# Kernel tuning notes

Hardware: AMD Instinct MI355X
Metric: run time of the kernel (lower is better)

The kernel has to match this reference:

```python
import jax, jax.numpy as jnp
import numpy as np

EPS = 1e-6
SCALING = 32 ** -0.5  # key_dim ** -0.5


def _ln(x, g, b):
    m = jnp.mean(x, -1, keepdims=True)
    v = jnp.var(x, -1, keepdims=True)
    return (x - m) * jax.lax.rsqrt(v + EPS) * g + b


def _dwconv(x, w, b, pad):
    # x: (B,H,W,C); w: (kh,kw,1,C) depthwise kernel
    y = jax.lax.conv_general_dilated(
        x, w, (1, 1), [(pad, pad), (pad, pad)],
        dimension_numbers=("NHWC", "HWIO", "NHWC"),
        feature_group_count=x.shape[-1])
    return y + b


def _rotate_every_two(x):
    x1 = x[..., ::2]
    x2 = x[..., 1::2]
    return jnp.stack([-x2, x1], axis=-1).reshape(x.shape)


def _theta_shift(x, sin, cos):
    return x * cos + _rotate_every_two(x) * sin


def setup_inputs() -> dict:
    key = jax.random.key(0)
    ks = jax.random.split(key, 32)
    B, H, W, C = 2, 56, 56, 256
    N, D = 8, C // 8          # heads, key_dim
    F = 1024                  # ffn_dim
    L = H * W
    g = 2 ** -2.5
    inp = {
        "x": jax.random.normal(ks[0], (B, H, W, C), jnp.float32),
        "sin": jax.random.normal(ks[1], (H, W, D), jnp.float32),
        "cos": jax.random.normal(ks[2], (H, W, D), jnp.float32),
        "mask": jax.random.normal(ks[3], (N, L, L), jnp.float32),
        # pos dwconv 3x3
        "pos_w": jax.random.normal(ks[4], (3, 3, 1, C), jnp.float32) * 0.05,
        "pos_b": jnp.zeros((C,), jnp.float32),
        # retention layernorm
        "ln1_g": jnp.ones((C,), jnp.float32),
        "ln1_b": jnp.zeros((C,), jnp.float32),
        # q/k/v projections (stored as (in,out))
        "wq": jax.random.normal(ks[5], (C, C), jnp.float32) * g * (2.0 / (C + C)) ** 0.5 * 10,
        "bq": jnp.zeros((C,), jnp.float32),
        "wk": jax.random.normal(ks[6], (C, C), jnp.float32) * g * 0.06,
        "bk": jnp.zeros((C,), jnp.float32),
        "wv": jax.random.normal(ks[7], (C, C), jnp.float32) * g * 0.06,
        "bv": jnp.zeros((C,), jnp.float32),
        # lepe dwconv 5x5
        "lepe_w": jax.random.normal(ks[8], (5, 5, 1, C), jnp.float32) * 0.05,
        "lepe_b": jnp.zeros((C,), jnp.float32),
        # out proj
        "wo": jax.random.normal(ks[9], (C, C), jnp.float32) * 0.06,
        "bo": jnp.zeros((C,), jnp.float32),
        # final layernorm
        "ln2_g": jnp.ones((C,), jnp.float32),
        "ln2_b": jnp.zeros((C,), jnp.float32),
        # ffn
        "w1": jax.random.normal(ks[10], (C, F), jnp.float32) * 0.04,
        "b1": jnp.zeros((F,), jnp.float32),
        "ffn_w": jax.random.normal(ks[11], (3, 3, 1, F), jnp.float32) * 0.05,
        "ffn_b": jnp.zeros((F,), jnp.float32),
        "w2": jax.random.normal(ks[12], (F, C), jnp.float32) * 0.04,
        "b2": jnp.zeros((C,), jnp.float32),
    }
    return inp


def _forward(x, sin, cos, mask, pos_w, pos_b, ln1_g, ln1_b, wq, bq, wk, bk,
             wv, bv, lepe_w, lepe_b, wo, bo, ln2_g, ln2_b, w1, b1,
             ffn_w, ffn_b, w2, b2):
    B, H, W, C = x.shape
    N = mask.shape[0]
    D = C // N
    L = H * W

    # positional dwconv residual
    x = x + _dwconv(x, pos_w, pos_b, 1)

    # ---- retention (VisionRetentionAll) ----
    y = _ln(x, ln1_g, ln1_b)
    q = y @ wq + bq
    k = (y @ wk + bk) * SCALING
    v = y @ wv + bv
    lepe = _dwconv(v, lepe_w, lepe_b, 2)

    # (B,H,W,C) -> (B,N,H,W,D)
    q = q.reshape(B, H, W, N, D).transpose(0, 3, 1, 2, 4)
    k = k.reshape(B, H, W, N, D).transpose(0, 3, 1, 2, 4)
    qr = _theta_shift(q, sin, cos).reshape(B, N, L, D)
    kr = _theta_shift(k, sin, cos).reshape(B, N, L, D)
    vr = v.reshape(B, H, W, N, D).transpose(0, 3, 1, 2, 4).reshape(B, N, L, D)

    qk = jnp.einsum("bnld,bnmd->bnlm", qr, kr) + mask  # (B,N,L,L)
    att = jax.nn.softmax(qk, axis=-1)
    out = jnp.einsum("bnlm,bnmd->bnld", att, vr)       # (B,N,L,D)
    out = out.transpose(0, 2, 1, 3).reshape(B, H, W, C)
    out = (out + lepe) @ wo + bo
    x = x + out

    # ---- FFN with depthwise conv ----
    z = _ln(x, ln2_g, ln2_b)
    z = jax.nn.gelu(z @ w1 + b1, approximate=False)
    z = z + _dwconv(z, ffn_w, ffn_b, 1)
    z = z @ w2 + b2
    return x + z


def reference(x, sin, cos, mask, pos_w, pos_b, ln1_g, ln1_b, wq, bq, wk, bk,
              wv, bv, lepe_w, lepe_b, wo, bo, ln2_g, ln2_b, w1, b1,
              ffn_w, ffn_b, w2, b2):
    return _forward(x, sin, cos, mask, pos_w, pos_b, ln1_g, ln1_b, wq, bq,
                    wk, bk, wv, bv, lepe_w, lepe_b, wo, bo, ln2_g, ln2_b,
                    w1, b1, ffn_w, ffn_b, w2, b2)
```

## Files before the change

kernel.cpp:

```cpp
#include <hip/hip_runtime.h>
#include <hip/hip_bf16.h>
#include <math.h>

#define Bn 2
#define Hn 56
#define Wn 56
#define Cn 256
#define Nh 8
#define Dh 32
#define Fn 1024
#define Ln (Hn*Wn)
#define Mrows (Bn*Ln)
#define SCALING_K 0.17677669529663687f

typedef __attribute__((ext_vector_type(4))) float f32x4;
typedef __attribute__((ext_vector_type(8))) short s16x8;
typedef unsigned short ushort_t;

__device__ __forceinline__ ushort_t f2bf(float f) {
    __hip_bfloat16 h = __float2bfloat16(f);
    return *reinterpret_cast<ushort_t*>(&h);
}

__global__ __launch_bounds__(256) void transpose_w(
    const float* __restrict__ wq, const float* __restrict__ wk, const float* __restrict__ wv,
    const float* __restrict__ wo, const float* __restrict__ w1, const float* __restrict__ w2,
    ushort_t* __restrict__ wqkvT, ushort_t* __restrict__ woT,
    ushort_t* __restrict__ w1T, ushort_t* __restrict__ w2T)
{
    int z = blockIdx.z;
    const float* src; ushort_t* dst; int K, N; float scale = 1.f;
    switch (z) {
      case 0: src=wq; dst=wqkvT;           K=256;  N=256;  break;
      case 1: src=wk; dst=wqkvT+256*256;   K=256;  N=256;  scale=SCALING_K; break;
      case 2: src=wv; dst=wqkvT+512*256;   K=256;  N=256;  break;
      case 3: src=wo; dst=woT;             K=256;  N=256;  break;
      case 4: src=w1; dst=w1T;             K=256;  N=1024; break;
      default: src=w2; dst=w2T;            K=1024; N=256;  break;
    }
    int n0 = blockIdx.x << 5, k0 = blockIdx.y << 5;
    if (n0 >= N || k0 >= K) return;
    __shared__ float tile[32][33];
    int tx = threadIdx.x & 31, ty = threadIdx.x >> 5;
    #pragma unroll
    for (int r = 0; r < 4; ++r)
        tile[ty + 8*r][tx] = src[(size_t)(k0 + ty + 8*r)*N + n0 + tx] * scale;
    __syncthreads();
    #pragma unroll
    for (int r = 0; r < 4; ++r)
        dst[(size_t)(n0 + ty + 8*r)*K + k0 + tx] = f2bf(tile[tx][ty + 8*r]);
}

__global__ void prep_bias(const float* __restrict__ bq, const float* __restrict__ bk,
                          const float* __restrict__ bv, float* __restrict__ bqkv)
{
    int i = blockIdx.x*256 + threadIdx.x;
    if (i < 768)
        bqkv[i] = (i < 256) ? bq[i] : (i < 512 ? bk[i-256]*SCALING_K : bv[i-512]);
}

__global__ __launch_bounds__(256) void dwconv_ln(
    const float* __restrict__ x, const float* __restrict__ wgt, const float* __restrict__ bias,
    float* __restrict__ out, float2* __restrict__ stats)
{
    int t = threadIdx.x;
    int cg = t & 63;
    int g = blockIdx.x*4 + (t >> 6);
    int w0 = (g % 14) << 2;
    int hr = g / 14;
    int h = hr % Hn;
    int c = cg << 2;
    float4 wv9[9];
    #pragma unroll
    for (int i = 0; i < 9; ++i) wv9[i] = *(const float4*)&wgt[i*Cn + c];
    float4 bias4 = *(const float4*)&bias[c];
    float4 acc[4] = {bias4, bias4, bias4, bias4};
    const float* base = x + (size_t)(hr - h)*Wn*Cn + c;
    #pragma unroll
    for (int dh = 0; dh < 3; ++dh) {
        int hh = h + dh - 1;
        if (hh < 0 || hh >= Hn) continue;
        const float* rowp = base + (size_t)hh*Wn*Cn;
        float4 xv[6];
        #pragma unroll
        for (int j = 0; j < 6; ++j) {
            int wc = w0 - 1 + j;
            xv[j] = (wc >= 0 && wc < Wn) ? *(const float4*)&rowp[(size_t)wc*Cn]
                                         : make_float4(0.f,0.f,0.f,0.f);
        }
        #pragma unroll
        for (int dw = 0; dw < 3; ++dw) {
            float4 wv = wv9[dh*3 + dw];
            #pragma unroll
            for (int p = 0; p < 4; ++p) {
                acc[p].x += xv[p+dw].x*wv.x; acc[p].y += xv[p+dw].y*wv.y;
                acc[p].z += xv[p+dw].z*wv.z; acc[p].w += xv[p+dw].w*wv.w;
            }
        }
        if (dh == 1) {
            #pragma unroll
            for (int p = 0; p < 4; ++p) {
                acc[p].x += xv[p+1].x; acc[p].y += xv[p+1].y;
                acc[p].z += xv[p+1].z; acc[p].w += xv[p+1].w;
            }
        }
    }
    float s[4], q[4];
    #pragma unroll
    for (int p = 0; p < 4; ++p) {
        s[p] = acc[p].x + acc[p].y + acc[p].z + acc[p].w;
        q[p] = acc[p].x*acc[p].x + acc[p].y*acc[p].y + acc[p].z*acc[p].z + acc[p].w*acc[p].w;
    }
    #pragma unroll
    for (int m = 1; m < 64; m <<= 1) {
        #pragma unroll
        for (int p = 0; p < 4; ++p) {
            s[p] += __shfl_xor(s[p], m);
            q[p] += __shfl_xor(q[p], m);
        }
    }
    size_t pixbase = (size_t)hr*Wn + w0;
    #pragma unroll
    for (int p = 0; p < 4; ++p)
        *(float4*)&out[(pixbase + p)*Cn + c] = acc[p];
    if (cg == 0) {
        #pragma unroll
        for (int p = 0; p < 4; ++p) {
            float mean = s[p] * (1.0f/Cn);
            float var  = q[p] * (1.0f/Cn) - mean*mean;
            stats[pixbase + p] = make_float2(mean, rsqrtf(var + 1e-6f));
        }
    }
}

template<int KS, int OBF>
__global__ __launch_bounds__(256) void dwconv4(
    const float* __restrict__ in, const float* __restrict__ wgt, const float* __restrict__ bias,
    void* __restrict__ outv, int C, int inld, int addin)
{
    constexpr int PAD = KS/2;
    int t = threadIdx.x;
    int cgs = C >> 2;
    int qpb = 256 / cgs;
    int cg = t % cgs;
    int g = blockIdx.x*qpb + t/cgs;
    int w0 = (g % 14) << 2;
    int hr = g / 14;
    int h = hr % Hn;
    int c = cg << 2;
    float4 bias4 = *(const float4*)&bias[c];
    float4 acc[4] = {bias4, bias4, bias4, bias4};
    const float* base = in + (size_t)(hr - h)*Wn*inld + c;
    #pragma unroll
    for (int dh = 0; dh < KS; ++dh) {
        int hh = h + dh - PAD;
        if (hh < 0 || hh >= Hn) continue;
        const float* rowp = base + (size_t)hh*Wn*inld;
        float4 xv[KS+3];
        #pragma unroll
        for (int j = 0; j < KS+3; ++j) {
            int wc = w0 - PAD + j;
            xv[j] = (wc >= 0 && wc < Wn) ? *(const float4*)&rowp[(size_t)wc*inld]
                                         : make_float4(0.f,0.f,0.f,0.f);
        }
        #pragma unroll
        for (int dw = 0; dw < KS; ++dw) {
            float4 wv = *(const float4*)&wgt[(dh*KS + dw)*C + c];
            #pragma unroll
            for (int p = 0; p < 4; ++p) {
                acc[p].x += xv[p+dw].x*wv.x; acc[p].y += xv[p+dw].y*wv.y;
                acc[p].z += xv[p+dw].z*wv.z; acc[p].w += xv[p+dw].w*wv.w;
            }
        }
        if (addin && dh == PAD) {
            #pragma unroll
            for (int p = 0; p < 4; ++p) {
                acc[p].x += xv[p+PAD].x; acc[p].y += xv[p+PAD].y;
                acc[p].z += xv[p+PAD].z; acc[p].w += xv[p+PAD].w;
            }
        }
    }
    size_t pixbase = (size_t)hr*Wn + w0;
    if (OBF) {
        ushort_t* outb = (ushort_t*)outv;
        #pragma unroll
        for (int p = 0; p < 4; ++p) {
            ushort_t tmp[4] = { f2bf(acc[p].x), f2bf(acc[p].y), f2bf(acc[p].z), f2bf(acc[p].w) };
            *(uint2*)&outb[(pixbase + p)*C + c] = *(uint2*)tmp;
        }
    } else {
        float* outf = (float*)outv;
        #pragma unroll
        for (int p = 0; p < 4; ++p)
            *(float4*)&outf[(pixbase + p)*C + c] = acc[p];
    }
}

__global__ __launch_bounds__(256) void ln_stats(const float* __restrict__ in, float2* __restrict__ stats)
{
    int row = blockIdx.x;
    int t = threadIdx.x;
    float v = in[(size_t)row*Cn + t];
    float s1 = v, s2 = v*v;
    #pragma unroll
    for (int m = 1; m < 64; m <<= 1) {
        s1 += __shfl_xor(s1, m);
        s2 += __shfl_xor(s2, m);
    }
    __shared__ float w1s[4], w2s[4];
    if ((t & 63) == 0) { w1s[t>>6] = s1; w2s[t>>6] = s2; }
    __syncthreads();
    if (t == 0) {
        s1 = w1s[0]+w1s[1]+w1s[2]+w1s[3];
        s2 = w2s[0]+w2s[1]+w2s[2]+w2s[3];
        float mean = s1 * (1.0f/Cn);
        float var  = s2 * (1.0f/Cn) - mean*mean;
        stats[row] = make_float2(mean, rsqrtf(var + 1e-6f));
    }
}

__global__ __launch_bounds__(256) void gemm_bf16(
    const void* __restrict__ Av, int abf16, const float* __restrict__ A2, int lda,
    const float2* __restrict__ lnstat, const float* __restrict__ lng, const float* __restrict__ lnb,
    const ushort_t* __restrict__ BT, const float* __restrict__ bias,
    const float* __restrict__ resid, float* __restrict__ out, int ldo,
    int K, int gelu_flag)
{
    __shared__ __align__(16) ushort_t As[64][40];
    __shared__ __align__(16) ushort_t Bs[64][40];
    int t = threadIdx.x;
    int wid = t >> 6, lane = t & 63, l16 = lane & 15, quad = lane >> 4;
    int n0 = blockIdx.x << 6, m0 = blockIdx.y << 6;
    int srow = t >> 2, skc = (t & 3) << 3;
    float2 st = make_float2(0.f, 1.f);
    if (lnstat) st = lnstat[m0 + srow];
    f32x4 acc[4] = {{0,0,0,0},{0,0,0,0},{0,0,0,0},{0,0,0,0}};
    for (int k0 = 0; k0 < K; k0 += 32) {
        ushort_t ac[8];
        if (abf16) {
            *(uint4*)ac = *(const uint4*)&((const ushort_t*)Av)[(size_t)(m0+srow)*lda + k0 + skc];
        } else {
            float av[8];
            const float* ap = &((const float*)Av)[(size_t)(m0+srow)*lda + k0 + skc];
            *(float4*)&av[0] = *(const float4*)ap;
            *(float4*)&av[4] = *(const float4*)(ap + 4);
            if (A2) {
                const float* ap2 = &A2[(size_t)(m0+srow)*lda + k0 + skc];
                float4 x0 = *(const float4*)ap2;
                float4 x1 = *(const float4*)(ap2 + 4);
                av[0]+=x0.x; av[1]+=x0.y; av[2]+=x0.z; av[3]+=x0.w;
                av[4]+=x1.x; av[5]+=x1.y; av[6]+=x1.z; av[7]+=x1.w;
            }
            if (lnstat) {
                float gg[8], bb[8];
                *(float4*)&gg[0] = *(const float4*)&lng[k0 + skc];
                *(float4*)&gg[4] = *(const float4*)&lng[k0 + skc + 4];
                *(float4*)&bb[0] = *(const float4*)&lnb[k0 + skc];
                *(float4*)&bb[4] = *(const float4*)&lnb[k0 + skc + 4];
                #pragma unroll
                for (int i = 0; i < 8; ++i)
                    av[i] = (av[i] - st.x)*st.y*gg[i] + bb[i];
            }
            #pragma unroll
            for (int i = 0; i < 8; ++i) ac[i] = f2bf(av[i]);
        }
        uint4 bv4 = *(const uint4*)&BT[(size_t)(n0+srow)*K + k0 + skc];
        __syncthreads();
        *(uint4*)&As[srow][skc] = *(uint4*)ac;
        *(uint4*)&Bs[srow][skc] = bv4;
        __syncthreads();
        s16x8 af = *(const s16x8*)&As[wid*16 + l16][quad*8];
        #pragma unroll
        for (int j = 0; j < 4; ++j) {
            s16x8 bf = *(const s16x8*)&Bs[j*16 + l16][quad*8];
            acc[j] = __builtin_amdgcn_mfma_f32_16x16x32_bf16(af, bf, acc[j], 0, 0, 0);
        }
    }
    #pragma unroll
    for (int j = 0; j < 4; ++j) {
        int col = n0 + j*16 + l16;
        float bv = bias[col];
        #pragma unroll
        for (int r = 0; r < 4; ++r) {
            int row = m0 + wid*16 + quad*4 + r;
            float v = acc[j][r] + bv;
            if (gelu_flag) v = 0.5f * v * (1.0f + erff(v * 0.70710678118654752f));
            size_t off = (size_t)row*ldo + col;
            if (resid) v += resid[off];
            out[off] = v;
        }
    }
}

__global__ __launch_bounds__(256) void pack_qkv(
    const float* __restrict__ qkv,
    const float* __restrict__ sp, const float* __restrict__ cp,
    ushort_t* __restrict__ qb, ushort_t* __restrict__ kb, ushort_t* __restrict__ vbT)
{
    __shared__ __align__(16) ushort_t Vl[64][40];
    int t = threadIdx.x;
    int l0 = blockIdx.x << 6;
    int n = blockIdx.y;
    int b = blockIdx.z;
    {
        int ll = t >> 2, dc = (t & 3) << 3;
        int l = l0 + ll;
        size_t gbase = ((size_t)(b*Ln + l))*768 + n*Dh + dc;
        float qx[8], kx[8], vx[8], sv[8], cv[8];
        *(float4*)&qx[0] = *(const float4*)&qkv[gbase];
        *(float4*)&qx[4] = *(const float4*)&qkv[gbase+4];
        *(float4*)&kx[0] = *(const float4*)&qkv[gbase+256];
        *(float4*)&kx[4] = *(const float4*)&qkv[gbase+260];
        *(float4*)&vx[0] = *(const float4*)&qkv[gbase+512];
        *(float4*)&vx[4] = *(const float4*)&qkv[gbase+516];
        size_t scb = (size_t)l*Dh + dc;
        *(float4*)&sv[0] = *(const float4*)&sp[scb];
        *(float4*)&sv[4] = *(const float4*)&sp[scb+4];
        *(float4*)&cv[0] = *(const float4*)&cp[scb];
        *(float4*)&cv[4] = *(const float4*)&cp[scb+4];
        ushort_t qo[8], ko[8], vo[8];
        #pragma unroll
        for (int j = 0; j < 8; j += 2) {
            float q0 = qx[j]*cv[j] - qx[j+1]*sv[j];
            float q1 = qx[j+1]*cv[j+1] + qx[j]*sv[j+1];
            float k0 = kx[j]*cv[j] - kx[j+1]*sv[j];
            float k1 = kx[j+1]*cv[j+1] + kx[j]*sv[j+1];
            qo[j] = f2bf(q0); qo[j+1] = f2bf(q1);
            ko[j] = f2bf(k0); ko[j+1] = f2bf(k1);
            vo[j] = f2bf(vx[j]); vo[j+1] = f2bf(vx[j+1]);
        }
        size_t hbase = ((size_t)((b*Nh + n)*Ln + l))*Dh + dc;
        *(uint4*)&qb[hbase] = *(uint4*)qo;
        *(uint4*)&kb[hbase] = *(uint4*)ko;
        *(uint4*)&Vl[ll][dc] = *(uint4*)vo;
    }
    __syncthreads();
    {
        int d = t >> 3, lc = (t & 7) << 3;
        ushort_t tmp[8];
        #pragma unroll
        for (int i = 0; i < 8; ++i) tmp[i] = Vl[lc + i][d];
        size_t tbase = ((size_t)((b*Nh + n)*Dh + d))*Ln + l0 + lc;
        *(uint4*)&vbT[tbase] = *(uint4*)tmp;
    }
}

__global__ __launch_bounds__(512) void flash_mfma(
    const ushort_t* __restrict__ qb, const ushort_t* __restrict__ kb,
    const ushort_t* __restrict__ vbT, const float* __restrict__ mask,
    float* __restrict__ out)
{
    __shared__ __align__(16) ushort_t Kt[2][64][40];
    __shared__ __align__(16) ushort_t Vt[2][32][72];
    __shared__ __align__(16) ushort_t Ps[8][16][72];
    int t = threadIdx.x;
    int wid = t >> 6, lane = t & 63, l16 = lane & 15, quad = lane >> 4;
    int bb = wid & 1, wq16 = wid >> 1;
    int l0 = blockIdx.x << 6;
    int n = blockIdx.y;

    const ushort_t* qbp = qb + ((size_t)(bb*Nh + n))*Ln*Dh;
    s16x8 qfrag = *(const s16x8*)(qbp + (size_t)(l0 + wq16*16 + l16)*Dh + quad*8);
    const float* mbase = mask + (size_t)n*Ln*Ln + (size_t)(l0 + wq16*16 + quad*4)*Ln;

    int sb   = t >> 8;
    int krow = (t >> 2) & 63, kkc = (t & 3) << 3;
    int vrow = (t >> 3) & 31, vkc = (t & 7) << 3;
    const ushort_t* kst = kb  + ((size_t)(sb*Nh + n))*Ln*Dh;
    const ushort_t* vst = vbT + ((size_t)((sb*Nh + n)*Dh + vrow))*Ln;

    f32x4 O0 = {0.f,0.f,0.f,0.f}, O1 = {0.f,0.f,0.f,0.f};
    float m_[4], l_[4];
    #pragma unroll
    for (int r = 0; r < 4; ++r) { m_[r] = -INFINITY; l_[r] = 0.f; }

    uint4 kreg = *(const uint4*)(kst + (size_t)krow*Dh + kkc);
    uint4 vreg = *(const uint4*)(vst + vkc);
    f32x4 c0, c1, c2, c3;
    #pragma unroll
    for (int r = 0; r < 4; ++r) {
        const float* mr = mbase + (size_t)r*Ln + l16;
        c0[r] = mr[0]; c1[r] = mr[16]; c2[r] = mr[32]; c3[r] = mr[48];
    }

    for (int m0 = 0; m0 < Ln; m0 += 64) {
        __syncthreads();
        *(uint4*)&Kt[sb][krow][kkc] = kreg;
        *(uint4*)&Vt[sb][vrow][vkc] = vreg;
        __syncthreads();

        int m1 = m0 + 64;
        uint4 krn = kreg, vrn = vreg;
        f32x4 d0 = c0, d1 = c1, d2 = c2, d3 = c3;
        if (m1 < Ln) {
            krn = *(const uint4*)(kst + (size_t)(m1 + krow)*Dh + kkc);
            vrn = *(const uint4*)(vst + m1 + vkc);
            #pragma unroll
            for (int r = 0; r < 4; ++r) {
                const float* mr = mbase + (size_t)r*Ln + m1 + l16;
                d0[r] = mr[0]; d1[r] = mr[16]; d2[r] = mr[32]; d3[r] = mr[48];
            }
        }

        f32x4 S[4];
        {
            s16x8 kf0 = *(const s16x8*)&Kt[bb][ 0 + l16][quad*8];
            s16x8 kf1 = *(const s16x8*)&Kt[bb][16 + l16][quad*8];
            s16x8 kf2 = *(const s16x8*)&Kt[bb][32 + l16][quad*8];
            s16x8 kf3 = *(const s16x8*)&Kt[bb][48 + l16][quad*8];
            S[0] = __builtin_amdgcn_mfma_f32_16x16x32_bf16(qfrag, kf0, c0, 0, 0, 0);
            S[1] = __builtin_amdgcn_mfma_f32_16x16x32_bf16(qfrag, kf1, c1, 0, 0, 0);
            S[2] = __builtin_amdgcn_mfma_f32_16x16x32_bf16(qfrag, kf2, c2, 0, 0, 0);
            S[3] = __builtin_amdgcn_mfma_f32_16x16x32_bf16(qfrag, kf3, c3, 0, 0, 0);
        }
        #pragma unroll
        for (int r = 0; r < 4; ++r) {
            float tm = fmaxf(fmaxf(S[0][r], S[1][r]), fmaxf(S[2][r], S[3][r]));
            tm = fmaxf(tm, __shfl_xor(tm, 1));
            tm = fmaxf(tm, __shfl_xor(tm, 2));
            tm = fmaxf(tm, __shfl_xor(tm, 4));
            tm = fmaxf(tm, __shfl_xor(tm, 8));
            float nm = fmaxf(m_[r], tm);
            float al = __expf(m_[r] - nm);
            m_[r] = nm;
            float p0 = __expf(S[0][r] - nm);
            float p1 = __expf(S[1][r] - nm);
            float p2 = __expf(S[2][r] - nm);
            float p3 = __expf(S[3][r] - nm);
            float ps = p0 + p1 + p2 + p3;
            ps += __shfl_xor(ps, 1); ps += __shfl_xor(ps, 2);
            ps += __shfl_xor(ps, 4); ps += __shfl_xor(ps, 8);
            l_[r] = l_[r]*al + ps;
            O0[r] *= al; O1[r] *= al;
            int rr = quad*4 + r;
            Ps[wid][rr][ 0 + l16] = f2bf(p0);
            Ps[wid][rr][16 + l16] = f2bf(p1);
            Ps[wid][rr][32 + l16] = f2bf(p2);
            Ps[wid][rr][48 + l16] = f2bf(p3);
        }
        #pragma unroll
        for (int kc = 0; kc < 2; ++kc) {
            s16x8 pf  = *(const s16x8*)&Ps[wid][l16][kc*32 + quad*8];
            s16x8 vf0 = *(const s16x8*)&Vt[bb][ 0 + l16][kc*32 + quad*8];
            s16x8 vf1 = *(const s16x8*)&Vt[bb][16 + l16][kc*32 + quad*8];
            O0 = __builtin_amdgcn_mfma_f32_16x16x32_bf16(pf, vf0, O0, 0, 0, 0);
            O1 = __builtin_amdgcn_mfma_f32_16x16x32_bf16(pf, vf1, O1, 0, 0, 0);
        }
        kreg = krn; vreg = vrn;
        c0 = d0; c1 = d1; c2 = d2; c3 = d3;
    }
    #pragma unroll
    for (int r = 0; r < 4; ++r) {
        float inv = 1.0f / l_[r];
        size_t row = (size_t)(bb*Ln + l0 + wq16*16 + quad*4 + r)*Cn + n*Dh;
        out[row + l16]      = O0[r] * inv;
        out[row + 16 + l16] = O1[r] * inv;
    }
}

extern "C" void kernel_launch(void* const* d_in, const int* in_sizes, int n_in,
                              void* d_out, int out_size, void* d_ws, size_t ws_size,
                              hipStream_t stream) {
    const float* x     = (const float*)d_in[0];
    const float* sinp  = (const float*)d_in[1];
    const float* cosp  = (const float*)d_in[2];
    const float* mask  = (const float*)d_in[3];
    const float* pos_w = (const float*)d_in[4];
    const float* pos_b = (const float*)d_in[5];
    const float* ln1_g = (const float*)d_in[6];
    const float* ln1_b = (const float*)d_in[7];
    const float* wq = (const float*)d_in[8];
    const float* bq = (const float*)d_in[9];
    const float* wk = (const float*)d_in[10];
    const float* bk = (const float*)d_in[11];
    const float* wv = (const float*)d_in[12];
    const float* bv = (const float*)d_in[13];
    const float* lepe_w = (const float*)d_in[14];
    const float* lepe_b = (const float*)d_in[15];
    const float* wo = (const float*)d_in[16];
    const float* bo = (const float*)d_in[17];
    const float* ln2_g = (const float*)d_in[18];
    const float* ln2_b = (const float*)d_in[19];
    const float* w1 = (const float*)d_in[20];
    const float* b1 = (const float*)d_in[21];
    const float* ffn_w = (const float*)d_in[22];
    const float* ffn_b = (const float*)d_in[23];
    const float* w2 = (const float*)d_in[24];
    const float* b2 = (const float*)d_in[25];

    float* ws = (float*)d_ws;
    const size_t MC = (size_t)Mrows*Cn;
    float* xbuf = ws;
    float* qkv  = ws + MC;
    float* lepe = ws + 4*MC;
    float* x2   = ws + 5*MC;
    float* att  = ws + 6*MC;
    float* z1   = ws + 7*MC;
    ushort_t* z2bf = (ushort_t*)(ws + 11*MC);
    ushort_t* qb   = (ushort_t*)(ws + 13*MC);
    ushort_t* kb   = (ushort_t*)(ws + 13*MC + MC/2);
    ushort_t* vbT  = (ushort_t*)(ws + 14*MC);
    float* wtb = ws + 14*MC + MC/2;
    ushort_t* wqkvT = (ushort_t*)wtb;
    ushort_t* woT   = (ushort_t*)(wtb + 98304);
    ushort_t* w1T   = (ushort_t*)(wtb + 131072);
    ushort_t* w2T   = (ushort_t*)(wtb + 262144);
    float*    bqkv  = wtb + 393216;
    float2*   stats1 = (float2*)(wtb + 394240);
    float2*   stats2 = (float2*)(wtb + 406784);
    float* outp = (float*)d_out;

    transpose_w<<<dim3(32,32,6), 256, 0, stream>>>(wq,wk,wv,wo,w1,w2, wqkvT,woT,w1T,w2T);
    prep_bias<<<3, 256, 0, stream>>>(bq,bk,bv,bqkv);
    dwconv_ln<<<Mrows/16, 256, 0, stream>>>(x, pos_w, pos_b, xbuf, stats1);
    gemm_bf16<<<dim3(12, Mrows/64), 256, 0, stream>>>(xbuf, 0, nullptr, Cn,
        stats1, ln1_g, ln1_b, wqkvT, bqkv, nullptr, qkv, 768, Cn, 0);
    pack_qkv<<<dim3(Ln/64, Nh, Bn), 256, 0, stream>>>(qkv, sinp, cosp, qb, kb, vbT);
    dwconv4<5,0><<<Mrows/16, 256, 0, stream>>>(qkv+512, lepe_w, lepe_b, lepe, Cn, 768, 0);
    flash_mfma<<<dim3(Ln/64, Nh), 512, 0, stream>>>(qb, kb, vbT, mask, att);
    gemm_bf16<<<dim3(4, Mrows/64), 256, 0, stream>>>(att, 0, lepe, Cn,
        nullptr, nullptr, nullptr, woT, bo, xbuf, x2, Cn, Cn, 0);
    ln_stats<<<Mrows, 256, 0, stream>>>(x2, stats2);
    gemm_bf16<<<dim3(16, Mrows/64), 256, 0, stream>>>(x2, 0, nullptr, Cn,
        stats2, ln2_g, ln2_b, w1T, b1, nullptr, z1, Fn, Cn, 1);
    dwconv4<3,1><<<Mrows/4, 256, 0, stream>>>(z1, ffn_w, ffn_b, z2bf, Fn, Fn, 1);
    gemm_bf16<<<dim3(4, Mrows/64), 256, 0, stream>>>(z2bf, 1, nullptr, Fn,
        nullptr, nullptr, nullptr, w2T, b2, x2, outp, Cn, Fn, 0);
}
```

Baseline: 655.3 us.

## Apply layernorm and lepe add upstream, feed GEMMs bf16 activations

The first layernorm is now applied inside the pos-dwconv kernel and the second in a new row kernel, both writing normalized bf16 activations. The flash attention epilogue adds lepe and stores bf16. The GEMM A-load path is therefore a plain bf16 copy with no per-tile LN math, fp32-to-bf16 conversion or second operand read. The workspace is repacked, with z1 aliasing the qkv region. This moves normalization work out of GEMM loops that recompute it for every N tile and halves A-side read traffic, at the cost of an extra bf16 write and read of each activation.

```diff
diff --git a/kernel.cpp b/kernel.cpp
--- a/kernel.cpp
+++ b/kernel.cpp
@@ -61,7 +61,8 @@
 
 __global__ __launch_bounds__(256) void dwconv_ln(
     const float* __restrict__ x, const float* __restrict__ wgt, const float* __restrict__ bias,
-    float* __restrict__ out, float2* __restrict__ stats)
+    const float* __restrict__ lng, const float* __restrict__ lnb,
+    float* __restrict__ out, ushort_t* __restrict__ ybf)
 {
     int t = threadIdx.x;
     int cg = t & 63;
@@ -119,17 +120,21 @@
             q[p] += __shfl_xor(q[p], m);
         }
     }
+    float4 g4 = *(const float4*)&lng[c];
+    float4 b4 = *(const float4*)&lnb[c];
     size_t pixbase = (size_t)hr*Wn + w0;
     #pragma unroll
-    for (int p = 0; p < 4; ++p)
+    for (int p = 0; p < 4; ++p) {
         *(float4*)&out[(pixbase + p)*Cn + c] = acc[p];
-    if (cg == 0) {
-        #pragma unroll
-        for (int p = 0; p < 4; ++p) {
-            float mean = s[p] * (1.0f/Cn);
-            float var  = q[p] * (1.0f/Cn) - mean*mean;
-            stats[pixbase + p] = make_float2(mean, rsqrtf(var + 1e-6f));
-        }
+        float mean = s[p] * (1.0f/Cn);
+        float rstd = rsqrtf(q[p] * (1.0f/Cn) - mean*mean + 1e-6f);
+        ushort_t o[4] = {
+            f2bf((acc[p].x - mean)*rstd*g4.x + b4.x),
+            f2bf((acc[p].y - mean)*rstd*g4.y + b4.y),
+            f2bf((acc[p].z - mean)*rstd*g4.z + b4.z),
+            f2bf((acc[p].w - mean)*rstd*g4.w + b4.w)
+        };
+        *(uint2*)&ybf[(pixbase + p)*Cn + c] = *(uint2*)o;
     }
 }
 
@@ -196,32 +201,37 @@
     }
 }
 
-__global__ __launch_bounds__(256) void ln_stats(const float* __restrict__ in, float2* __restrict__ stats)
-{
-    int row = blockIdx.x;
+__global__ __launch_bounds__(256) void ln_apply(
+    const float* __restrict__ in, const float* __restrict__ g, const float* __restrict__ b,
+    ushort_t* __restrict__ out)
+{
     int t = threadIdx.x;
-    float v = in[(size_t)row*Cn + t];
-    float s1 = v, s2 = v*v;
+    int lane = t & 63;
+    int row = blockIdx.x*4 + (t >> 6);
+    int c = lane << 2;
+    float4 v = *(const float4*)&in[(size_t)row*Cn + c];
+    float s1 = v.x + v.y + v.z + v.w;
+    float s2 = v.x*v.x + v.y*v.y + v.z*v.z + v.w*v.w;
     #pragma unroll
     for (int m = 1; m < 64; m <<= 1) {
         s1 += __shfl_xor(s1, m);
         s2 += __shfl_xor(s2, m);
     }
-    __shared__ float w1s[4], w2s[4];
-    if ((t & 63) == 0) { w1s[t>>6] = s1; w2s[t>>6] = s2; }
-    __syncthreads();
-    if (t == 0) {
-        s1 = w1s[0]+w1s[1]+w1s[2]+w1s[3];
-        s2 = w2s[0]+w2s[1]+w2s[2]+w2s[3];
-        float mean = s1 * (1.0f/Cn);
-        float var  = s2 * (1.0f/Cn) - mean*mean;
-        stats[row] = make_float2(mean, rsqrtf(var + 1e-6f));
-    }
+    float mean = s1 * (1.0f/Cn);
+    float rstd = rsqrtf(s2 * (1.0f/Cn) - mean*mean + 1e-6f);
+    float4 g4 = *(const float4*)&g[c];
+    float4 b4 = *(const float4*)&b[c];
+    ushort_t o[4] = {
+        f2bf((v.x - mean)*rstd*g4.x + b4.x),
+        f2bf((v.y - mean)*rstd*g4.y + b4.y),
+        f2bf((v.z - mean)*rstd*g4.z + b4.z),
+        f2bf((v.w - mean)*rstd*g4.w + b4.w)
+    };
+    *(uint2*)&out[(size_t)row*Cn + c] = *(uint2*)o;
 }
 
 __global__ __launch_bounds__(256) void gemm_bf16(
-    const void* __restrict__ Av, int abf16, const float* __restrict__ A2, int lda,
-    const float2* __restrict__ lnstat, const float* __restrict__ lng, const float* __restrict__ lnb,
+    const ushort_t* __restrict__ A, int lda,
     const ushort_t* __restrict__ BT, const float* __restrict__ bias,
     const float* __restrict__ resid, float* __restrict__ out, int ldo,
     int K, int gelu_flag)
@@ -232,41 +242,12 @@
     int wid = t >> 6, lane = t & 63, l16 = lane & 15, quad = lane >> 4;
     int n0 = blockIdx.x << 6, m0 = blockIdx.y << 6;
     int srow = t >> 2, skc = (t & 3) << 3;
-    float2 st = make_float2(0.f, 1.f);
-    if (lnstat) st = lnstat[m0 + srow];
     f32x4 acc[4] = {{0,0,0,0},{0,0,0,0},{0,0,0,0},{0,0,0,0}};
     for (int k0 = 0; k0 < K; k0 += 32) {
-        ushort_t ac[8];
-        if (abf16) {
-            *(uint4*)ac = *(const uint4*)&((const ushort_t*)Av)[(size_t)(m0+srow)*lda + k0 + skc];
-        } else {
-            float av[8];
-            const float* ap = &((const float*)Av)[(size_t)(m0+srow)*lda + k0 + skc];
-            *(float4*)&av[0] = *(const float4*)ap;
-            *(float4*)&av[4] = *(const float4*)(ap + 4);
-            if (A2) {
-                const float* ap2 = &A2[(size_t)(m0+srow)*lda + k0 + skc];
-                float4 x0 = *(const float4*)ap2;
-                float4 x1 = *(const float4*)(ap2 + 4);
-                av[0]+=x0.x; av[1]+=x0.y; av[2]+=x0.z; av[3]+=x0.w;
-                av[4]+=x1.x; av[5]+=x1.y; av[6]+=x1.z; av[7]+=x1.w;
-            }
-            if (lnstat) {
-                float gg[8], bb[8];
-                *(float4*)&gg[0] = *(const float4*)&lng[k0 + skc];
-                *(float4*)&gg[4] = *(const float4*)&lng[k0 + skc + 4];
-                *(float4*)&bb[0] = *(const float4*)&lnb[k0 + skc];
-                *(float4*)&bb[4] = *(const float4*)&lnb[k0 + skc + 4];
-                #pragma unroll
-                for (int i = 0; i < 8; ++i)
-                    av[i] = (av[i] - st.x)*st.y*gg[i] + bb[i];
-            }
-            #pragma unroll
-            for (int i = 0; i < 8; ++i) ac[i] = f2bf(av[i]);
-        }
+        uint4 av4 = *(const uint4*)&A[(size_t)(m0+srow)*lda + k0 + skc];
         uint4 bv4 = *(const uint4*)&BT[(size_t)(n0+srow)*K + k0 + skc];
         __syncthreads();
-        *(uint4*)&As[srow][skc] = *(uint4*)ac;
+        *(uint4*)&As[srow][skc] = av4;
         *(uint4*)&Bs[srow][skc] = bv4;
         __syncthreads();
         s16x8 af = *(const s16x8*)&As[wid*16 + l16][quad*8];
@@ -348,7 +329,7 @@
 __global__ __launch_bounds__(512) void flash_mfma(
     const ushort_t* __restrict__ qb, const ushort_t* __restrict__ kb,
     const ushort_t* __restrict__ vbT, const float* __restrict__ mask,
-    float* __restrict__ out)
+    const float* __restrict__ lepe, ushort_t* __restrict__ out)
 {
     __shared__ __align__(16) ushort_t Kt[2][64][40];
     __shared__ __align__(16) ushort_t Vt[2][32][72];
@@ -453,8 +434,8 @@
     for (int r = 0; r < 4; ++r) {
         float inv = 1.0f / l_[r];
         size_t row = (size_t)(bb*Ln + l0 + wq16*16 + quad*4 + r)*Cn + n*Dh;
-        out[row + l16]      = O0[r] * inv;
-        out[row + 16 + l16] = O1[r] * inv;
+        out[row + l16]      = f2bf(O0[r] * inv + lepe[row + l16]);
+        out[row + 16 + l16] = f2bf(O1[r] * inv + lepe[row + 16 + l16]);
     }
 }
 
@@ -490,40 +471,41 @@
 
     float* ws = (float*)d_ws;
     const size_t MC = (size_t)Mrows*Cn;
+    const size_t HC = MC/2;
     float* xbuf = ws;
-    float* qkv  = ws + MC;
-    float* lepe = ws + 4*MC;
-    float* x2   = ws + 5*MC;
-    float* att  = ws + 6*MC;
-    float* z1   = ws + 7*MC;
-    ushort_t* z2bf = (ushort_t*)(ws + 11*MC);
-    ushort_t* qb   = (ushort_t*)(ws + 13*MC);
-    ushort_t* kb   = (ushort_t*)(ws + 13*MC + MC/2);
-    ushort_t* vbT  = (ushort_t*)(ws + 14*MC);
-    float* wtb = ws + 14*MC + MC/2;
+    float* x2   = ws + MC;
+    float* lepe = ws + 2*MC;
+    ushort_t* ybf   = (ushort_t*)(ws + 3*MC);
+    ushort_t* attbf = (ushort_t*)(ws + 3*MC + HC);
+    ushort_t* zbf   = (ushort_t*)(ws + 4*MC);
+    float* qkv = ws + 4*MC + HC;
+    ushort_t* qb  = (ushort_t*)(ws + 7*MC + HC);
+    ushort_t* kb  = (ushort_t*)(ws + 8*MC);
+    ushort_t* vbT = (ushort_t*)(ws + 8*MC + HC);
+    float* z1 = ws + 4*MC + HC;
+    ushort_t* z2bf = (ushort_t*)(ws + 9*MC);
+    float* wtb = ws + 11*MC;
     ushort_t* wqkvT = (ushort_t*)wtb;
     ushort_t* woT   = (ushort_t*)(wtb + 98304);
     ushort_t* w1T   = (ushort_t*)(wtb + 131072);
     ushort_t* w2T   = (ushort_t*)(wtb + 262144);
     float*    bqkv  = wtb + 393216;
-    float2*   stats1 = (float2*)(wtb + 394240);
-    float2*   stats2 = (float2*)(wtb + 406784);
     float* outp = (float*)d_out;
 
     transpose_w<<<dim3(32,32,6), 256, 0, stream>>>(wq,wk,wv,wo,w1,w2, wqkvT,woT,w1T,w2T);
     prep_bias<<<3, 256, 0, stream>>>(bq,bk,bv,bqkv);
-    dwconv_ln<<<Mrows/16, 256, 0, stream>>>(x, pos_w, pos_b, xbuf, stats1);
-    gemm_bf16<<<dim3(12, Mrows/64), 256, 0, stream>>>(xbuf, 0, nullptr, Cn,
-        stats1, ln1_g, ln1_b, wqkvT, bqkv, nullptr, qkv, 768, Cn, 0);
+    dwconv_ln<<<Mrows/16, 256, 0, stream>>>(x, pos_w, pos_b, ln1_g, ln1_b, xbuf, ybf);
+    gemm_bf16<<<dim3(12, Mrows/64), 256, 0, stream>>>(ybf, Cn,
+        wqkvT, bqkv, nullptr, qkv, 768, Cn, 0);
     pack_qkv<<<dim3(Ln/64, Nh, Bn), 256, 0, stream>>>(qkv, sinp, cosp, qb, kb, vbT);
     dwconv4<5,0><<<Mrows/16, 256, 0, stream>>>(qkv+512, lepe_w, lepe_b, lepe, Cn, 768, 0);
-    flash_mfma<<<dim3(Ln/64, Nh), 512, 0, stream>>>(qb, kb, vbT, mask, att);
-    gemm_bf16<<<dim3(4, Mrows/64), 256, 0, stream>>>(att, 0, lepe, Cn,
-        nullptr, nullptr, nullptr, woT, bo, xbuf, x2, Cn, Cn, 0);
-    ln_stats<<<Mrows, 256, 0, stream>>>(x2, stats2);
-    gemm_bf16<<<dim3(16, Mrows/64), 256, 0, stream>>>(x2, 0, nullptr, Cn,
-        stats2, ln2_g, ln2_b, w1T, b1, nullptr, z1, Fn, Cn, 1);
+    flash_mfma<<<dim3(Ln/64, Nh), 512, 0, stream>>>(qb, kb, vbT, mask, lepe, attbf);
+    gemm_bf16<<<dim3(4, Mrows/64), 256, 0, stream>>>(attbf, Cn,
+        woT, bo, xbuf, x2, Cn, Cn, 0);
+    ln_apply<<<Mrows/4, 256, 0, stream>>>(x2, ln2_g, ln2_b, zbf);
+    gemm_bf16<<<dim3(16, Mrows/64), 256, 0, stream>>>(zbf, Cn,
+        w1T, b1, nullptr, z1, Fn, Cn, 1);
     dwconv4<3,1><<<Mrows/4, 256, 0, stream>>>(z1, ffn_w, ffn_b, z2bf, Fn, Fn, 1);
-    gemm_bf16<<<dim3(4, Mrows/64), 256, 0, stream>>>(z2bf, 1, nullptr, Fn,
-        nullptr, nullptr, nullptr, w2T, b2, x2, outp, Cn, Fn, 0);
-}
+    gemm_bf16<<<dim3(4, Mrows/64), 256, 0, stream>>>(z2bf, Fn,
+        w2T, b2, x2, outp, Cn, Fn, 0);
+}
```

Measured after the change: 637.0 us. 2.8% less time.
